# Performance work log

Hardware: AMD Instinct MI355X
Metric: run time of the kernel (lower is better)

## Reference

```python
import jax, jax.numpy as jnp
import numpy as np

B, N, D, H = 512, 129, 256, 8   # batch, nodes (128 customers + depot), d_model, heads
HD = D // H                      # head_depth = 32
T = 128                          # decode steps
CLIP = 10.0                      # tanh_clipping
CAP = 1.0                        # VRPproblem.VEHICLE_CAPACITY


def setup_inputs() -> dict:
    key = jax.random.key(0)
    ks = jax.random.split(key, 9)
    s = 1.0 / np.sqrt(D)  # dense-layer init scale, keeps tanh logits unsaturated
    return {
        "embeddings": jax.random.normal(ks[0], (B, N, D), jnp.float32),
        "context_vectors": jax.random.normal(ks[1], (B, D), jnp.float32),
        "demands": jax.random.uniform(ks[2], (B, N), jnp.float32) * 0.1,
        "Wq_context": jax.random.normal(ks[3], (D, D), jnp.float32) * s,
        "Wq_step": jax.random.normal(ks[4], (D + 1, D), jnp.float32) * s,
        "Wk": jax.random.normal(ks[5], (D, D), jnp.float32) * s,
        "Wk_tanh": jax.random.normal(ks[6], (D, D), jnp.float32) * s,
        "Wv": jax.random.normal(ks[7], (D, D), jnp.float32) * s,
        "Wo": jax.random.normal(ks[8], (D, D), jnp.float32) * s,
    }


def _decode(embeddings, context_vectors, demands, Wq_context, Wq_step, Wk, Wk_tanh, Wv, Wo):
    b, n, dm = embeddings.shape
    hd = dm // H
    neg_inf = jnp.float32(-jnp.inf)
    # Precomputed once per rollout (as in the original call())
    K = (embeddings @ Wk).reshape(b, n, H, hd).transpose(0, 2, 1, 3)    # [b,H,n,hd]
    V = (embeddings @ Wv).reshape(b, n, H, hd).transpose(0, 2, 1, 3)    # [b,H,n,hd]
    Kt = embeddings @ Wk_tanh                                            # [b,n,dm]
    Qc = context_vectors @ Wq_context                                    # [b,dm]
    node_ids = jnp.arange(n)

    def step(carry, _):
        prev, used, visited = carry  # [b] int32, [b] f32, [b,n] bool (True = masked)
        # get_step_context: gather prev-node embedding, append remaining capacity
        cur = jnp.take_along_axis(embeddings, prev[:, None, None], axis=1)[:, 0]  # [b,dm]
        ctx = jnp.concatenate([cur, CAP - used[:, None]], axis=-1)                # [b,dm+1]
        Q = (Qc + ctx @ Wq_step).reshape(b, H, hd)                                # split heads, seq=1
        # decoder_mha: note original divides by head_depth (not sqrt)
        compat = jnp.einsum('bhd,bhnd->bhn', Q, K) / jnp.float32(hd)
        compat = jnp.where(visited[:, None, :], neg_inf, compat)
        attn = jnp.einsum('bhn,bhnd->bhd', jax.nn.softmax(compat, axis=-1), V)
        glimpse = attn.reshape(b, dm) @ Wo                                        # w_out
        # get_log_p: tanh-clipped pointer logits over all nodes
        logits = jnp.tanh(jnp.einsum('bd,bnd->bn', glimpse, Kt) / jnp.sqrt(jnp.float32(dm))) * CLIP
        logits = jnp.where(visited, neg_inf, logits)
        log_p = jax.nn.log_softmax(logits, axis=-1)                               # [b,n]
        # greedy _select_node + clip to valid range
        sel = jnp.clip(jnp.argmax(log_p, axis=-1).astype(jnp.int32), 0, n - 1)
        # state.step: visit node (depot index 0 always stays feasible), capacity update
        dem = jnp.take_along_axis(demands, sel[:, None], axis=1)[:, 0]
        used2 = jnp.where(sel == 0, jnp.float32(0.0), used + dem)
        visited2 = jnp.where(node_ids[None, :] == sel[:, None], sel[:, None] != 0, visited)
        return (sel, used2, visited2), (log_p, sel)

    init = (jnp.zeros((b,), jnp.int32), jnp.zeros((b,), jnp.float32), jnp.zeros((b, n), bool))
    _, (lp, pi) = jax.lax.scan(step, init, None, length=T)
    return lp.transpose(1, 0, 2), pi.T  # [b,T,n], [b,T]


def reference(embeddings, context_vectors, demands, Wq_context, Wq_step, Wk, Wk_tanh, Wv, Wo):
    log_probs, pi = _decode(embeddings, context_vectors, demands,
                            Wq_context, Wq_step, Wk, Wk_tanh, Wv, Wo)
    return log_probs, pi.astype(jnp.float32)
```

## Files before the change

### kernel.cpp

```cpp
#include <hip/hip_runtime.h>
#include <math.h>

#define NB 512
#define NN 129
#define DMM 256
#define NH 8
#define HDm 32
#define TT 128

#define PI_OFF ((size_t)NB * TT * NN)

#define NEG_SENTINEL (-1.0e30f)

#define EQ_SZ ((size_t)NB * NN * DMM)
#define V_OFF (EQ_SZ)
#define W2_OFF (2 * EQ_SZ)
#define QC_OFF (2 * EQ_SZ + (size_t)DMM * DMM)

__device__ __forceinline__ float tanh_fast(float x) {
  return 1.0f - 2.0f / (__expf(2.0f * x) + 1.0f);
}

__global__ __launch_bounds__(256) void w2_kernel(const float* __restrict__ Wkt,
                                                 const float* __restrict__ Wo,
                                                 float* __restrict__ W2) {
  __shared__ __align__(16) float rowL[DMM];
  int d = blockIdx.x, i = threadIdx.x;
  rowL[i] = Wkt[d * DMM + i];
  __syncthreads();
  const float4* wo4 = (const float4*)(Wo + (size_t)i * DMM);
  const float4* r4 = (const float4*)rowL;
  float acc = 0.f;
  #pragma unroll 8
  for (int jq = 0; jq < DMM / 4; ++jq) {
    float4 a = r4[jq], bq = wo4[jq];
    acc += a.x * bq.x + a.y * bq.y + a.z * bq.z + a.w * bq.w;
  }
  W2[d * DMM + i] = acc;
}

__global__ __launch_bounds__(256) void qc_kernel(const float* __restrict__ ctx,
                                                 const float* __restrict__ Wqc,
                                                 float* __restrict__ Qc) {
  __shared__ __align__(16) float cL[DMM];
  int b = blockIdx.x, j = threadIdx.x;
  cL[j] = ctx[b * DMM + j];
  __syncthreads();
  float acc = 0.f;
  for (int i = 0; i < DMM; ++i) acc += cL[i] * Wqc[i * DMM + j];
  Qc[b * DMM + j] = acc;
}

__global__ __launch_bounds__(256) void eqv_kernel(const float* __restrict__ emb,
                                                  const float* __restrict__ Wqs,
                                                  const float* __restrict__ Wv,
                                                  float* __restrict__ Eq,
                                                  float* __restrict__ Vws) {
  __shared__ __align__(16) float eL[64][DMM];
  int j = threadIdx.x;
  size_t r0 = (size_t)blockIdx.x * 64;
  for (int k = 0; k < 64; ++k) eL[k][j] = emb[(r0 + k) * DMM + j];
  __syncthreads();
  float accE[64], accV[64];
  #pragma unroll
  for (int r = 0; r < 64; ++r) { accE[r] = 0.f; accV[r] = 0.f; }
  for (int iq = 0; iq < 64; ++iq) {
    float we[4], wv[4];
    #pragma unroll
    for (int k = 0; k < 4; ++k) {
      we[k] = Wqs[(iq * 4 + k) * DMM + j];
      wv[k] = Wv[(iq * 4 + k) * DMM + j];
    }
    #pragma unroll
    for (int r = 0; r < 64; ++r) {
      float4 e = *(const float4*)&eL[r][iq * 4];
      accE[r] += e.x * we[0] + e.y * we[1] + e.z * we[2] + e.w * we[3];
      accV[r] += e.x * wv[0] + e.y * wv[1] + e.z * wv[2] + e.w * wv[3];
    }
  }
  for (int r = 0; r < 64; ++r) {
    Eq[(r0 + r) * DMM + j] = accE[r];
    Vws[(r0 + r) * DMM + j] = accV[r];
  }
}

__global__ __launch_bounds__(512, 2) void decode_kernel(
    const float* __restrict__ emb, const float* __restrict__ demands,
    const float* __restrict__ Wk, const float* __restrict__ Wqs,
    const float* __restrict__ Eq, const float* __restrict__ W2,
    const float* __restrict__ Qc, const float* __restrict__ Vws,
    float* __restrict__ out) {
  extern __shared__ float sm[];
  float* K128L = sm;
  float* T128L = sm + 256;
  float* V128L = sm + 512;
  float* demL = sm + 768;
  float* SCR = sm + 904;
  float* SCR2 = SCR + 33156;
  float* embL = SCR;
  float* WkT = SCR2;
  float* W2T = SCR2 + 2048;
  float* qL = SCR2;
  float* pm = SCR2 + 256;
  float* attnL = SCR2 + 1312;
  float* ypd = SCR2 + 1568;

  const int tid = threadIdx.x;
  const int b = blockIdx.x;
  const int w = tid >> 6;
  const int l = tid & 63;
  const int dv = l & 31, h2 = l >> 5;

  const float* embB = emb + (size_t)b * NN * DMM;

  for (int idx = tid; idx < NN * DMM; idx += 512) {
    int r = idx >> 8, c = idx & 255;
    embL[r * 257 + c] = embB[idx];
  }
  if (tid < 132) demL[tid] = (tid < NN) ? demands[b * NN + tid] : 0.f;
  __syncthreads();

  if (tid < 256) {
    float a0 = 0.f, a1 = 0.f;
    for (int i = 0; i < DMM; ++i) {
      float e = embL[128 * 257 + i];
      a0 += e * Wk[i * DMM + tid];
      a1 += e * W2[i * DMM + tid];
    }
    K128L[tid] = a0;
    T128L[tid] = a1;
    V128L[tid] = Vws[((size_t)b * NN + 128) * DMM + tid];
  }

  float Kr0[HDm], Kr1[HDm], Tr0[HDm], Tr1[HDm];
  #pragma unroll
  for (int d = 0; d < HDm; ++d) { Kr0[d] = 0.f; Kr1[d] = 0.f; Tr0[d] = 0.f; Tr1[d] = 0.f; }
  for (int it = 0; it < 32; ++it) {
    __syncthreads();
    for (int idx = tid; idx < 2048; idx += 512) {
      WkT[idx] = Wk[it * 2048 + idx];
      W2T[idx] = W2[it * 2048 + idx];
    }
    __syncthreads();
    for (int i = 0; i < 8; ++i) {
      float e0 = embL[l * 257 + it * 8 + i];
      float e1 = embL[(l + 64) * 257 + it * 8 + i];
      const float4* wk4 = (const float4*)(WkT + i * DMM + w * HDm);
      const float4* w24 = (const float4*)(W2T + i * DMM + w * HDm);
      #pragma unroll
      for (int c = 0; c < 8; ++c) {
        float4 kv = wk4[c], tv = w24[c];
        Kr0[4*c+0] += e0 * kv.x; Kr0[4*c+1] += e0 * kv.y; Kr0[4*c+2] += e0 * kv.z; Kr0[4*c+3] += e0 * kv.w;
        Kr1[4*c+0] += e1 * kv.x; Kr1[4*c+1] += e1 * kv.y; Kr1[4*c+2] += e1 * kv.z; Kr1[4*c+3] += e1 * kv.w;
        Tr0[4*c+0] += e0 * tv.x; Tr0[4*c+1] += e0 * tv.y; Tr0[4*c+2] += e0 * tv.z; Tr0[4*c+3] += e0 * tv.w;
        Tr1[4*c+0] += e1 * tv.x; Tr1[4*c+1] += e1 * tv.y; Tr1[4*c+2] += e1 * tv.z; Tr1[4*c+3] += e1 * tv.w;
      }
    }
  }

  float Vr[64];
  {
    const float* vb = Vws + ((size_t)b * NN + h2 * 64) * DMM + w * HDm + dv;
    #pragma unroll
    for (int jj = 0; jj < 64; ++jj) Vr[jj] = vb[(size_t)jj * DMM];
  }

  float qcR = Qc[b * DMM + w * HDm + dv];
  float wqR = Wqs[256 * DMM + w * HDm + dv];
  float eqR = Eq[((size_t)b * NN + 0) * DMM + w * HDm + dv];

  float used = 0.f;
  int vis0 = 0, vis1 = 0, vis128 = 0;
  float pa = 0.f, pb = 0.f, pc = 0.f;
  __syncthreads();

  float* outB = out + (size_t)b * TT * NN;

  for (int t = 0; t < TT; ++t) {
    float qd = qcR + eqR + (1.0f - used) * wqR;
    if (l < 32) qL[w * HDm + l] = qd;

    if (t > 0) {
      float ta = (pa == -INFINITY) ? -INFINITY : 10.f * tanh_fast(pa * 0.0625f);
      float tb = (pb == -INFINITY) ? -INFINITY : 10.f * tanh_fast(pb * 0.0625f);
      float tc = (l == 0 && pc != -INFINITY) ? 10.f * tanh_fast(pc * 0.0625f)
                                             : -INFINITY;
      float ea = __expf(ta), eb = __expf(tb);
      float ec = (l == 0) ? __expf(tc) : 0.f;
      float se = ea + eb + ec;
      #pragma unroll
      for (int o = 32; o > 0; o >>= 1) se += __shfl_xor(se, o);
      float lse = __logf(se);
      float* op = outB + (size_t)(t - 1) * NN;
      if (w < 4) {
        if ((l >> 4) == w) op[l] = fmaxf(ta - lse, NEG_SENTINEL);
      } else {
        if ((l >> 4) == w - 4) op[l + 64] = fmaxf(tb - lse, NEG_SENTINEL);
      }
      if (w == 0 && l == 0) op[128] = fmaxf(tc - lse, NEG_SENTINEL);
    }

    float s0, s1, s2;
    {
      const float4* q4 = (const float4*)(qL + w * HDm);
      const float4* k4 = (const float4*)(K128L + w * HDm);
      float a0 = 0.f, a1 = 0.f, a2 = 0.f, a3 = 0.f;
      float b0 = 0.f, b1 = 0.f, b2 = 0.f, b3 = 0.f;
      float c0 = 0.f, c1 = 0.f, c2 = 0.f, c3 = 0.f;
      #pragma unroll
      for (int c = 0; c < 8; ++c) {
        float4 q = q4[c], k = k4[c];
        a0 += q.x * Kr0[4*c];   a1 += q.y * Kr0[4*c+1];
        a2 += q.z * Kr0[4*c+2]; a3 += q.w * Kr0[4*c+3];
        b0 += q.x * Kr1[4*c];   b1 += q.y * Kr1[4*c+1];
        b2 += q.z * Kr1[4*c+2]; b3 += q.w * Kr1[4*c+3];
        c0 += q.x * k.x; c1 += q.y * k.y; c2 += q.z * k.z; c3 += q.w * k.w;
      }
      s0 = ((a0 + a1) + (a2 + a3)) * 0.03125f;
      s1 = ((b0 + b1) + (b2 + b3)) * 0.03125f;
      s2 = ((c0 + c1) + (c2 + c3)) * 0.03125f;
    }
    if (vis0) s0 = -INFINITY;
    if (vis1) s1 = -INFINITY;
    float e0 = __expf(s0), e1 = __expf(s1);
    float e2 = (l == 0 && !vis128) ? __expf(s2) : 0.f;
    pm[w * 132 + l] = e0;
    pm[w * 132 + 64 + l] = e1;
    if (l == 0) pm[w * 132 + 128] = e2;
    float psum = e0 + e1 + e2;

    float acc;
    {
      const float4* pr = (const float4*)(pm + w * 132 + h2 * 64);
      float a0 = 0.f, a1 = 0.f, a2 = 0.f, a3 = 0.f;
      #pragma unroll
      for (int jq = 0; jq < 16; ++jq) {
        float4 p4 = pr[jq];
        a0 += p4.x * Vr[4*jq];   a1 += p4.y * Vr[4*jq+1];
        a2 += p4.z * Vr[4*jq+2]; a3 += p4.w * Vr[4*jq+3];
      }
      acc = (a0 + a1) + (a2 + a3);
    }
    if (h2 == 0) acc += pm[w * 132 + 128] * V128L[w * HDm + dv];
    acc += __shfl_xor(acc, 32);
    if (l < 32) attnL[w * HDm + l] = acc;
    #pragma unroll
    for (int o = 32; o > 0; o >>= 1) psum += __shfl_xor(psum, o);
    float inv = 1.0f / psum;

    float* ypb = ypd + (t & 1) * 1056;
    float y0, y1;
    {
      const float4* a4 = (const float4*)(attnL + w * HDm);
      float a0 = 0.f, a1 = 0.f, a2 = 0.f, a3 = 0.f;
      float b0 = 0.f, b1 = 0.f, b2 = 0.f, b3 = 0.f;
      #pragma unroll
      for (int c = 0; c < 8; ++c) {
        float4 a = a4[c];
        a0 += a.x * Tr0[4*c];   a1 += a.y * Tr0[4*c+1];
        a2 += a.z * Tr0[4*c+2]; a3 += a.w * Tr0[4*c+3];
        b0 += a.x * Tr1[4*c];   b1 += a.y * Tr1[4*c+1];
        b2 += a.z * Tr1[4*c+2]; b3 += a.w * Tr1[4*c+3];
      }
      y0 = ((a0 + a1) + (a2 + a3)) * inv;
      y1 = ((b0 + b1) + (b2 + b3)) * inv;
    }
    ypb[w * 132 + l] = y0;
    ypb[w * 132 + 64 + l] = y1;
    {
      float yy = 0.f;
      if (l < 8) {
        float4 a = ((const float4*)(attnL + w * HDm))[l];
        float4 tq = ((const float4*)(T128L + w * HDm))[l];
        yy = a.x * tq.x + a.y * tq.y + a.z * tq.z + a.w * tq.w;
      }
      yy += __shfl_xor(yy, 4);
      yy += __shfl_xor(yy, 2);
      yy += __shfl_xor(yy, 1);
      if (l == 0) ypb[w * 132 + 128] = yy * inv;
    }

    __syncthreads();

    const float* yp = ypd + (t & 1) * 1056;
    float ya = 0.f, yb = 0.f, ys = 0.f;
    #pragma unroll
    for (int ww = 0; ww < 8; ++ww) {
      ya += yp[ww * 132 + l];
      yb += yp[ww * 132 + 64 + l];
      ys += yp[ww * 132 + 128];
    }
    float ra = vis0 ? -INFINITY : ya;
    float rb = vis1 ? -INFINITY : yb;
    float rc = (l == 0 && !vis128) ? ys : -INFINITY;

    float mx = fmaxf(fmaxf(ra, rb), rc);
    #pragma unroll
    for (int o = 32; o > 0; o >>= 1) mx = fmaxf(mx, __shfl_xor(mx, o));
    unsigned long long ba = __ballot(ra == mx);
    unsigned long long bb = __ballot(rb == mx);
    int sel = ba ? (__ffsll((long long)ba) - 1)
                 : (bb ? 64 + (__ffsll((long long)bb) - 1) : 128);

    float eqNew = Eq[((size_t)b * NN + sel) * DMM + w * HDm + dv];
    float dmv = demL[sel];
    if (w == 0 && l == 0) out[PI_OFF + (size_t)b * TT + t] = (float)sel;

    pa = ra; pb = rb; pc = rc;

    used = (sel == 0) ? 0.f : used + dmv;
    if (sel == l && sel != 0) vis0 = 1;
    if (sel == l + 64) vis1 = 1;
    if (sel == 128) vis128 = 1;
    eqR = eqNew;
  }

  {
    float ta = (pa == -INFINITY) ? -INFINITY : 10.f * tanh_fast(pa * 0.0625f);
    float tb = (pb == -INFINITY) ? -INFINITY : 10.f * tanh_fast(pb * 0.0625f);
    float tc = (l == 0 && pc != -INFINITY) ? 10.f * tanh_fast(pc * 0.0625f)
                                           : -INFINITY;
    float ea = __expf(ta), eb = __expf(tb);
    float ec = (l == 0) ? __expf(tc) : 0.f;
    float se = ea + eb + ec;
    #pragma unroll
    for (int o = 32; o > 0; o >>= 1) se += __shfl_xor(se, o);
    float lse = __logf(se);
    float* op = outB + (size_t)(TT - 1) * NN;
    if (w < 4) {
      if ((l >> 4) == w) op[l] = fmaxf(ta - lse, NEG_SENTINEL);
    } else {
      if ((l >> 4) == w - 4) op[l + 64] = fmaxf(tb - lse, NEG_SENTINEL);
    }
    if (w == 0 && l == 0) op[128] = fmaxf(tc - lse, NEG_SENTINEL);
  }
}

extern "C" void kernel_launch(void* const* d_in, const int* in_sizes, int n_in,
                              void* d_out, int out_size, void* d_ws, size_t ws_size,
                              hipStream_t stream) {
  const float* emb = (const float*)d_in[0];
  const float* ctx = (const float*)d_in[1];
  const float* dem = (const float*)d_in[2];
  const float* Wqc = (const float*)d_in[3];
  const float* Wqs = (const float*)d_in[4];
  const float* Wk = (const float*)d_in[5];
  const float* Wkt = (const float*)d_in[6];
  const float* Wv = (const float*)d_in[7];
  const float* Wo = (const float*)d_in[8];
  float* out = (float*)d_out;
  float* ws = (float*)d_ws;

  float* Eq = ws;
  float* Vws = ws + V_OFF;
  float* W2 = ws + W2_OFF;
  float* Qc = ws + QC_OFF;

  w2_kernel<<<dim3(DMM), dim3(DMM), 0, stream>>>(Wkt, Wo, W2);
  qc_kernel<<<dim3(NB), dim3(DMM), 0, stream>>>(ctx, Wqc, Qc);
  eqv_kernel<<<dim3((NB * NN) / 64), dim3(256), 0, stream>>>(emb, Wqs, Wv, Eq, Vws);

  const int SMEM = 38156 * 4;
  hipFuncSetAttribute(reinterpret_cast<const void*>(decode_kernel),
                      hipFuncAttributeMaxDynamicSharedMemorySize, SMEM);
  decode_kernel<<<dim3(NB), dim3(512), SMEM, stream>>>(emb, dem, Wk, Wqs, Eq, W2, Qc,
                                                       Vws, out);
}
```

Baseline: 1.354 ms.

## Split each head across two waves with 1024-thread blocks and shrink LDS

Each head is now split across two wavefronts, each covering 64 nodes. The block grows to 1024 threads, and per-thread K, T and V register arrays are halved. The full per-batch embedding is no longer staged in shared memory; an 8-column slice is streamed per projection iteration, which cuts dynamic LDS from about 150KB to about 25KB so more blocks can be resident per CU. The cost is an extra __syncthreads per decode step to combine the partial attention sums of the two waves, plus a launch-bounds hint that may tightly constrain register allocation and cause spills.

```diff
diff --git a/kernel.cpp b/kernel.cpp
--- a/kernel.cpp
+++ b/kernel.cpp
@@ -84,7 +84,7 @@
   }
 }
 
-__global__ __launch_bounds__(512, 2) void decode_kernel(
+__global__ __launch_bounds__(1024, 4) void decode_kernel(
     const float* __restrict__ emb, const float* __restrict__ demands,
     const float* __restrict__ Wk, const float* __restrict__ Wqs,
     const float* __restrict__ Eq, const float* __restrict__ W2,
@@ -95,35 +95,36 @@
   float* T128L = sm + 256;
   float* V128L = sm + 512;
   float* demL = sm + 768;
-  float* SCR = sm + 904;
-  float* SCR2 = SCR + 33156;
-  float* embL = SCR;
-  float* WkT = SCR2;
-  float* W2T = SCR2 + 2048;
+  float* SCR2 = sm + 904;
+  float* embT = SCR2;
+  float* WkT = SCR2 + 1168;
+  float* W2T = SCR2 + 3216;
+  float* row128L = SCR2 + 5264;
   float* qL = SCR2;
-  float* pm = SCR2 + 256;
-  float* attnL = SCR2 + 1312;
-  float* ypd = SCR2 + 1568;
+  float* pm = SCR2 + 512;
+  float* attnP = SCR2 + 1568;
+  float* psumP = SCR2 + 2080;
+  float* ypd = SCR2 + 2096;
 
   const int tid = threadIdx.x;
   const int b = blockIdx.x;
   const int w = tid >> 6;
+  const int h = w >> 1;
+  const int p = w & 1;
   const int l = tid & 63;
   const int dv = l & 31, h2 = l >> 5;
+  const int nl = p * 64 + l;
 
   const float* embB = emb + (size_t)b * NN * DMM;
 
-  for (int idx = tid; idx < NN * DMM; idx += 512) {
-    int r = idx >> 8, c = idx & 255;
-    embL[r * 257 + c] = embB[idx];
-  }
+  if (tid < 256) row128L[tid] = embB[128 * DMM + tid];
   if (tid < 132) demL[tid] = (tid < NN) ? demands[b * NN + tid] : 0.f;
   __syncthreads();
 
   if (tid < 256) {
     float a0 = 0.f, a1 = 0.f;
     for (int i = 0; i < DMM; ++i) {
-      float e = embL[128 * 257 + i];
+      float e = row128L[i];
       a0 += e * Wk[i * DMM + tid];
       a1 += e * W2[i * DMM + tid];
     }
@@ -132,42 +133,41 @@
     V128L[tid] = Vws[((size_t)b * NN + 128) * DMM + tid];
   }
 
-  float Kr0[HDm], Kr1[HDm], Tr0[HDm], Tr1[HDm];
+  float Kr[HDm], Tr[HDm];
   #pragma unroll
-  for (int d = 0; d < HDm; ++d) { Kr0[d] = 0.f; Kr1[d] = 0.f; Tr0[d] = 0.f; Tr1[d] = 0.f; }
+  for (int d = 0; d < HDm; ++d) { Kr[d] = 0.f; Tr[d] = 0.f; }
   for (int it = 0; it < 32; ++it) {
     __syncthreads();
-    for (int idx = tid; idx < 2048; idx += 512) {
-      WkT[idx] = Wk[it * 2048 + idx];
-      W2T[idx] = W2[it * 2048 + idx];
-    }
+    WkT[tid] = Wk[it * 2048 + tid];
+    WkT[tid + 1024] = Wk[it * 2048 + tid + 1024];
+    W2T[tid] = W2[it * 2048 + tid];
+    W2T[tid + 1024] = W2[it * 2048 + tid + 1024];
+    embT[(tid >> 3) * 9 + (tid & 7)] = embB[(tid >> 3) * DMM + it * 8 + (tid & 7)];
     __syncthreads();
     for (int i = 0; i < 8; ++i) {
-      float e0 = embL[l * 257 + it * 8 + i];
-      float e1 = embL[(l + 64) * 257 + it * 8 + i];
-      const float4* wk4 = (const float4*)(WkT + i * DMM + w * HDm);
-      const float4* w24 = (const float4*)(W2T + i * DMM + w * HDm);
+      float e = embT[nl * 9 + i];
+      const float4* wk4 = (const float4*)(WkT + i * DMM + h * HDm);
+      const float4* w24 = (const float4*)(W2T + i * DMM + h * HDm);
       #pragma unroll
       for (int c = 0; c < 8; ++c) {
         float4 kv = wk4[c], tv = w24[c];
-        Kr0[4*c+0] += e0 * kv.x; Kr0[4*c+1] += e0 * kv.y; Kr0[4*c+2] += e0 * kv.z; Kr0[4*c+3] += e0 * kv.w;
-        Kr1[4*c+0] += e1 * kv.x; Kr1[4*c+1] += e1 * kv.y; Kr1[4*c+2] += e1 * kv.z; Kr1[4*c+3] += e1 * kv.w;
-        Tr0[4*c+0] += e0 * tv.x; Tr0[4*c+1] += e0 * tv.y; Tr0[4*c+2] += e0 * tv.z; Tr0[4*c+3] += e0 * tv.w;
-        Tr1[4*c+0] += e1 * tv.x; Tr1[4*c+1] += e1 * tv.y; Tr1[4*c+2] += e1 * tv.z; Tr1[4*c+3] += e1 * tv.w;
-      }
-    }
-  }
-
-  float Vr[64];
+        Kr[4*c+0] += e * kv.x; Kr[4*c+1] += e * kv.y; Kr[4*c+2] += e * kv.z; Kr[4*c+3] += e * kv.w;
+        Tr[4*c+0] += e * tv.x; Tr[4*c+1] += e * tv.y; Tr[4*c+2] += e * tv.z; Tr[4*c+3] += e * tv.w;
+      }
+    }
+  }
+
+  float Vr[HDm];
   {
-    const float* vb = Vws + ((size_t)b * NN + h2 * 64) * DMM + w * HDm + dv;
-    #pragma unroll
-    for (int jj = 0; jj < 64; ++jj) Vr[jj] = vb[(size_t)jj * DMM];
-  }
-
-  float qcR = Qc[b * DMM + w * HDm + dv];
-  float wqR = Wqs[256 * DMM + w * HDm + dv];
-  float eqR = Eq[((size_t)b * NN + 0) * DMM + w * HDm + dv];
+    const float* vb = Vws + ((size_t)b * NN + p * 64 + h2 * 32) * DMM + h * HDm + dv;
+    #pragma unroll
+    for (int jj = 0; jj < HDm; ++jj) Vr[jj] = vb[(size_t)jj * DMM];
+  }
+
+  float qcR = Qc[b * DMM + h * HDm + dv];
+  float wqR = Wqs[256 * DMM + h * HDm + dv];
+  float eqR = Eq[((size_t)b * NN + 0) * DMM + h * HDm + dv];
+  const float* eqPtr = Eq + (size_t)b * NN * DMM + h * HDm + dv;
 
   float used = 0.f;
   int vis0 = 0, vis1 = 0, vis128 = 0;
@@ -178,7 +178,7 @@
 
   for (int t = 0; t < TT; ++t) {
     float qd = qcR + eqR + (1.0f - used) * wqR;
-    if (l < 32) qL[w * HDm + l] = qd;
+    if (h2 == 0) qL[w * HDm + dv] = qd;
 
     if (t > 0) {
       float ta = (pa == -INFINITY) ? -INFINITY : 10.f * tanh_fast(pa * 0.0625f);
@@ -192,103 +192,104 @@
       for (int o = 32; o > 0; o >>= 1) se += __shfl_xor(se, o);
       float lse = __logf(se);
       float* op = outB + (size_t)(t - 1) * NN;
-      if (w < 4) {
-        if ((l >> 4) == w) op[l] = fmaxf(ta - lse, NEG_SENTINEL);
+      if (w < 8) {
+        if ((l >> 3) == w) op[l] = fmaxf(ta - lse, NEG_SENTINEL);
       } else {
-        if ((l >> 4) == w - 4) op[l + 64] = fmaxf(tb - lse, NEG_SENTINEL);
+        if ((l >> 3) == w - 8) op[l + 64] = fmaxf(tb - lse, NEG_SENTINEL);
       }
       if (w == 0 && l == 0) op[128] = fmaxf(tc - lse, NEG_SENTINEL);
     }
 
-    float s0, s1, s2;
+    float s;
     {
       const float4* q4 = (const float4*)(qL + w * HDm);
-      const float4* k4 = (const float4*)(K128L + w * HDm);
       float a0 = 0.f, a1 = 0.f, a2 = 0.f, a3 = 0.f;
-      float b0 = 0.f, b1 = 0.f, b2 = 0.f, b3 = 0.f;
+      #pragma unroll
+      for (int c = 0; c < 8; ++c) {
+        float4 q = q4[c];
+        a0 += q.x * Kr[4*c];   a1 += q.y * Kr[4*c+1];
+        a2 += q.z * Kr[4*c+2]; a3 += q.w * Kr[4*c+3];
+      }
+      s = ((a0 + a1) + (a2 + a3)) * 0.03125f;
+    }
+    if (p ? vis1 : vis0) s = -INFINITY;
+    float e0 = __expf(s);
+    pm[h * 132 + nl] = e0;
+    float e2 = 0.f;
+    if (p == 0) {
+      const float4* q4 = (const float4*)(qL + w * HDm);
+      const float4* k4 = (const float4*)(K128L + h * HDm);
       float c0 = 0.f, c1 = 0.f, c2 = 0.f, c3 = 0.f;
       #pragma unroll
       for (int c = 0; c < 8; ++c) {
         float4 q = q4[c], k = k4[c];
-        a0 += q.x * Kr0[4*c];   a1 += q.y * Kr0[4*c+1];
-        a2 += q.z * Kr0[4*c+2]; a3 += q.w * Kr0[4*c+3];
-        b0 += q.x * Kr1[4*c];   b1 += q.y * Kr1[4*c+1];
-        b2 += q.z * Kr1[4*c+2]; b3 += q.w * Kr1[4*c+3];
         c0 += q.x * k.x; c1 += q.y * k.y; c2 += q.z * k.z; c3 += q.w * k.w;
       }
-      s0 = ((a0 + a1) + (a2 + a3)) * 0.03125f;
-      s1 = ((b0 + b1) + (b2 + b3)) * 0.03125f;
-      s2 = ((c0 + c1) + (c2 + c3)) * 0.03125f;
-    }
-    if (vis0) s0 = -INFINITY;
-    if (vis1) s1 = -INFINITY;
-    float e0 = __expf(s0), e1 = __expf(s1);
-    float e2 = (l == 0 && !vis128) ? __expf(s2) : 0.f;
-    pm[w * 132 + l] = e0;
-    pm[w * 132 + 64 + l] = e1;
-    if (l == 0) pm[w * 132 + 128] = e2;
-    float psum = e0 + e1 + e2;
+      float s2 = ((c0 + c1) + (c2 + c3)) * 0.03125f;
+      float e2l = vis128 ? 0.f : __expf(s2);
+      if (l == 0) { pm[h * 132 + 128] = e2l; e2 = e2l; }
+    }
+    float psum = e0 + e2;
+    #pragma unroll
+    for (int o = 32; o > 0; o >>= 1) psum += __shfl_xor(psum, o);
+    if (l == 0) psumP[w] = psum;
 
     float acc;
     {
-      const float4* pr = (const float4*)(pm + w * 132 + h2 * 64);
+      const float4* pr = (const float4*)(pm + h * 132 + p * 64 + h2 * 32);
       float a0 = 0.f, a1 = 0.f, a2 = 0.f, a3 = 0.f;
       #pragma unroll
-      for (int jq = 0; jq < 16; ++jq) {
+      for (int jq = 0; jq < 8; ++jq) {
         float4 p4 = pr[jq];
         a0 += p4.x * Vr[4*jq];   a1 += p4.y * Vr[4*jq+1];
         a2 += p4.z * Vr[4*jq+2]; a3 += p4.w * Vr[4*jq+3];
       }
       acc = (a0 + a1) + (a2 + a3);
     }
-    if (h2 == 0) acc += pm[w * 132 + 128] * V128L[w * HDm + dv];
+    if (p == 0 && h2 == 0) acc += pm[h * 132 + 128] * V128L[h * HDm + dv];
     acc += __shfl_xor(acc, 32);
-    if (l < 32) attnL[w * HDm + l] = acc;
-    #pragma unroll
-    for (int o = 32; o > 0; o >>= 1) psum += __shfl_xor(psum, o);
-    float inv = 1.0f / psum;
-
-    float* ypb = ypd + (t & 1) * 1056;
-    float y0, y1;
+    if (h2 == 0) attnP[w * HDm + dv] = acc;
+
+    __syncthreads();
+
+    float inv = 1.0f / (psumP[2 * h] + psumP[2 * h + 1]);
+    float y;
     {
-      const float4* a4 = (const float4*)(attnL + w * HDm);
+      const float4* aA = (const float4*)(attnP + (2 * h) * HDm);
+      const float4* aB = (const float4*)(attnP + (2 * h + 1) * HDm);
       float a0 = 0.f, a1 = 0.f, a2 = 0.f, a3 = 0.f;
-      float b0 = 0.f, b1 = 0.f, b2 = 0.f, b3 = 0.f;
       #pragma unroll
       for (int c = 0; c < 8; ++c) {
-        float4 a = a4[c];
-        a0 += a.x * Tr0[4*c];   a1 += a.y * Tr0[4*c+1];
-        a2 += a.z * Tr0[4*c+2]; a3 += a.w * Tr0[4*c+3];
-        b0 += a.x * Tr1[4*c];   b1 += a.y * Tr1[4*c+1];
-        b2 += a.z * Tr1[4*c+2]; b3 += a.w * Tr1[4*c+3];
-      }
-      y0 = ((a0 + a1) + (a2 + a3)) * inv;
-      y1 = ((b0 + b1) + (b2 + b3)) * inv;
-    }
-    ypb[w * 132 + l] = y0;
-    ypb[w * 132 + 64 + l] = y1;
-    {
+        float4 u = aA[c], v = aB[c];
+        a0 += (u.x + v.x) * Tr[4*c];   a1 += (u.y + v.y) * Tr[4*c+1];
+        a2 += (u.z + v.z) * Tr[4*c+2]; a3 += (u.w + v.w) * Tr[4*c+3];
+      }
+      y = ((a0 + a1) + (a2 + a3)) * inv;
+    }
+    ypd[h * 132 + nl] = y;
+    if (p == 0) {
       float yy = 0.f;
       if (l < 8) {
-        float4 a = ((const float4*)(attnL + w * HDm))[l];
-        float4 tq = ((const float4*)(T128L + w * HDm))[l];
-        yy = a.x * tq.x + a.y * tq.y + a.z * tq.z + a.w * tq.w;
+        float4 u = ((const float4*)(attnP + (2 * h) * HDm))[l];
+        float4 v = ((const float4*)(attnP + (2 * h + 1) * HDm))[l];
+        float4 tq = ((const float4*)(T128L + h * HDm))[l];
+        yy = (u.x + v.x) * tq.x + (u.y + v.y) * tq.y +
+             (u.z + v.z) * tq.z + (u.w + v.w) * tq.w;
       }
       yy += __shfl_xor(yy, 4);
       yy += __shfl_xor(yy, 2);
       yy += __shfl_xor(yy, 1);
-      if (l == 0) ypb[w * 132 + 128] = yy * inv;
+      if (l == 0) ypd[h * 132 + 128] = yy * inv;
     }
 
     __syncthreads();
 
-    const float* yp = ypd + (t & 1) * 1056;
     float ya = 0.f, yb = 0.f, ys = 0.f;
     #pragma unroll
-    for (int ww = 0; ww < 8; ++ww) {
-      ya += yp[ww * 132 + l];
-      yb += yp[ww * 132 + 64 + l];
-      ys += yp[ww * 132 + 128];
+    for (int hh = 0; hh < 8; ++hh) {
+      ya += ypd[hh * 132 + l];
+      yb += ypd[hh * 132 + 64 + l];
+      ys += ypd[hh * 132 + 128];
     }
     float ra = vis0 ? -INFINITY : ya;
     float rb = vis1 ? -INFINITY : yb;
@@ -302,7 +303,7 @@
     int sel = ba ? (__ffsll((long long)ba) - 1)
                  : (bb ? 64 + (__ffsll((long long)bb) - 1) : 128);
 
-    float eqNew = Eq[((size_t)b * NN + sel) * DMM + w * HDm + dv];
+    float eqNew = eqPtr[(size_t)sel * DMM];
     float dmv = demL[sel];
     if (w == 0 && l == 0) out[PI_OFF + (size_t)b * TT + t] = (float)sel;
 
@@ -327,10 +328,10 @@
     for (int o = 32; o > 0; o >>= 1) se += __shfl_xor(se, o);
     float lse = __logf(se);
     float* op = outB + (size_t)(TT - 1) * NN;
-    if (w < 4) {
-      if ((l >> 4) == w) op[l] = fmaxf(ta - lse, NEG_SENTINEL);
+    if (w < 8) {
+      if ((l >> 3) == w) op[l] = fmaxf(ta - lse, NEG_SENTINEL);
     } else {
-      if ((l >> 4) == w - 4) op[l + 64] = fmaxf(tb - lse, NEG_SENTINEL);
+      if ((l >> 3) == w - 8) op[l + 64] = fmaxf(tb - lse, NEG_SENTINEL);
     }
     if (w == 0 && l == 0) op[128] = fmaxf(tc - lse, NEG_SENTINEL);
   }
@@ -360,9 +361,9 @@
   qc_kernel<<<dim3(NB), dim3(DMM), 0, stream>>>(ctx, Wqc, Qc);
   eqv_kernel<<<dim3((NB * NN) / 64), dim3(256), 0, stream>>>(emb, Wqs, Wv, Eq, Vws);
 
-  const int SMEM = 38156 * 4;
+  const int SMEM = 6432 * 4;
   hipFuncSetAttribute(reinterpret_cast<const void*>(decode_kernel),
                       hipFuncAttributeMaxDynamicSharedMemorySize, SMEM);
-  decode_kernel<<<dim3(NB), dim3(512), SMEM, stream>>>(emb, dem, Wk, Wqs, Eq, W2, Qc,
-                                                       Vws, out);
-}
+  decode_kernel<<<dim3(NB), dim3(1024), SMEM, stream>>>(emb, dem, Wk, Wqs, Eq, W2,
+                                                        Qc, Vws, out);
+}
```

Result: slower. 3.198 ms (+136.3%).
